# Kernel optimization log

Hardware: AMD Instinct MI355X
Metric: run time of the kernel (lower is better)

Reference implementation:

```python
import jax, jax.numpy as jnp
import numpy as np

N = 100000   # nodes
E = 1600000  # edges (avg degree 16)
D = 64       # input_dim
H = 64       # hidden_dim
C = 40       # num_classes
K = 2        # x_steps (KProp)


def setup_inputs() -> dict:
    key = jax.random.key(0)
    ks = jax.random.split(key, 8)
    x = jax.random.normal(ks[0], (N, D), dtype=jnp.float32)
    edge_src = jax.random.randint(ks[1], (E,), 0, N, dtype=jnp.int32)
    edge_dst = jax.random.randint(ks[2], (E,), 0, N, dtype=jnp.int32)
    def lin(k, fi, fo):
        b = 1.0 / np.sqrt(fi)
        return jax.random.uniform(k, (fi, fo), jnp.float32, -b, b)
    Wl1 = lin(ks[3], D, H)  # SAGEConv1 neighbor weight
    Wr1 = lin(ks[4], D, H)  # SAGEConv1 root weight
    b1 = jnp.zeros((H,), jnp.float32)
    Wl2 = lin(ks[5], H, C)
    Wr2 = lin(ks[6], H, C)
    b2 = jnp.zeros((C,), jnp.float32)
    return {"x": x, "Wl1": Wl1, "Wr1": Wr1, "b1": b1,
            "Wl2": Wl2, "Wr2": Wr2, "b2": b2,
            "edge_src": edge_src, "edge_dst": edge_dst}


def reference(x, Wl1, Wr1, b1, Wl2, Wr2, b2, edge_src, edge_dst):
    ones = jnp.ones((edge_src.shape[0],), x.dtype)
    deg = jax.ops.segment_sum(ones, edge_dst, num_segments=N)  # in-degree (adj_t row sums)
    # gcn_norm without self loops: w_e = deg[dst]^-1/2 * deg[src]^-1/2 (inf -> 0)
    dis = jnp.where(deg > 0, jax.lax.rsqrt(jnp.maximum(deg, 1.0)), 0.0)
    w = dis[edge_dst] * dis[edge_src]
    # KProp: K steps of normalized sparse matmul, 'add' aggregation
    h = x
    for _ in range(K):
        h = jax.ops.segment_sum(h[edge_src] * w[:, None], edge_dst, num_segments=N)
    cnt = jnp.maximum(deg, 1.0)[:, None]  # mean-aggr denominator (0-row safe)
    # SAGEConv1: lin_l(mean_neighbors) + lin_r(root), then selu (dropout p=0)
    agg1 = jax.ops.segment_sum(h[edge_src], edge_dst, num_segments=N) / cnt
    h1 = jax.nn.selu(agg1 @ Wl1 + h @ Wr1 + b1)
    # SAGEConv2
    agg2 = jax.ops.segment_sum(h1[edge_src], edge_dst, num_segments=N) / cnt
    out = agg2 @ Wl2 + h1 @ Wr2 + b2
    return jax.nn.softmax(out, axis=1)
```

## Files before the change

kernel.cpp:

```cpp
#include <hip/hip_runtime.h>
#include <hip/hip_bf16.h>
#include <math.h>


#define RFL(x) __builtin_amdgcn_readfirstlane(x)
#define BK_SHIFT 10
#define MAXBUCK 256

typedef short bf16x8 __attribute__((ext_vector_type(8)));
typedef _Float16 f16x8 __attribute__((ext_vector_type(8)));
typedef float f32x4 __attribute__((ext_vector_type(4)));
typedef unsigned short ushort8v __attribute__((ext_vector_type(8)));

__device__ __forceinline__ float bf2f(unsigned short u) {
    return __uint_as_float((unsigned)u << 16);
}
__device__ __forceinline__ unsigned short f2bf(float f) {
    __hip_bfloat16 b = __float2bfloat16(f);
    return *reinterpret_cast<unsigned short*>(&b);
}
__device__ __forceinline__ unsigned short f2h(float f) {
    _Float16 h = (_Float16)f;
    return *reinterpret_cast<unsigned short*>(&h);
}


__global__ __launch_bounds__(256) void partition_kernel(const int* __restrict__ src,
                                                        const int* __restrict__ dst,
                                                        int* __restrict__ bcursor,
                                                        unsigned int* __restrict__ temp,
                                                        int e, int nbuck, int cap) {
    __shared__ int bc[MAXBUCK];
    int t = threadIdx.x;
    int chunk = (e + gridDim.x - 1) / gridDim.x;
    int base = blockIdx.x * chunk;
    int cnt = e - base;
    if (cnt > chunk) cnt = chunk;
    if (cnt < 0) cnt = 0;
    for (int j = t; j < nbuck; j += 256) bc[j] = 0;
    __syncthreads();
    for (int i = t; i < cnt; i += 256) {
        int d = dst[base + i];
        atomicAdd(&bc[d >> BK_SHIFT], 1);
    }
    __syncthreads();
    for (int j = t; j < nbuck; j += 256) {
        int c = bc[j];
        bc[j] = (c > 0) ? (atomicAdd(&bcursor[j], c) + j * cap) : 0;
    }
    __syncthreads();
    for (int i = t; i < cnt; i += 256) {
        int s = src[base + i];
        int d = dst[base + i];
        int bk = d >> BK_SHIFT;
        int p = atomicAdd(&bc[bk], 1);
        if (p < (bk + 1) * cap) temp[p] = ((unsigned int)s << BK_SHIFT) | (unsigned int)(d & 1023);
    }
}

__global__ __launch_bounds__(256) void bucket_csr_kernel(const unsigned int* __restrict__ temp,
                                                         const int* __restrict__ bcursor,
                                                         int* __restrict__ row_ptr,
                                                         float* __restrict__ dis,
                                                         float* __restrict__ cnt_inv,
                                                         int* __restrict__ csr_src,
                                                         int n, int cap, int nbuck, int e) {
    __shared__ int cnt3[1024];
    __shared__ int part[256];
    int b = blockIdx.x;
    int t = threadIdx.x;
    int nbeg = b << BK_SHIFT;
    int cj = 0;
    if (t < nbuck) {
        cj = bcursor[t];
        if (cj > cap) cj = cap;
    }
    part[t] = cj;
    __syncthreads();
    for (int off = 1; off < 256; off <<= 1) {
        int u = (t >= off) ? part[t - off] : 0;
        __syncthreads();
        part[t] += u;
        __syncthreads();
    }
    int cntb = bcursor[b];
    if (cntb > cap) cntb = cap;
    int bbase = part[b] - cntb;
    __syncthreads();
    for (int i = t; i < 1024; i += 256) cnt3[i] = 0;
    __syncthreads();
    const unsigned int* tb = temp + (size_t)b * cap;
    for (int i = t; i < cntb; i += 256) {
        atomicAdd(&cnt3[tb[i] & 1023u], 1);
    }
    __syncthreads();
    int d0 = cnt3[t * 4 + 0], d1 = cnt3[t * 4 + 1], d2 = cnt3[t * 4 + 2], d3 = cnt3[t * 4 + 3];
    int run = d0 + d1 + d2 + d3;
    int dd[4] = {d0, d1, d2, d3};
#pragma unroll
    for (int k = 0; k < 4; ++k) {
        int node = nbeg + t * 4 + k;
        if (node < n) {
            float fd = (float)dd[k];
            dis[node] = (dd[k] > 0) ? rsqrtf(fd) : 0.0f;
            cnt_inv[node] = 1.0f / fmaxf(fd, 1.0f);
        }
    }
    __syncthreads();
    part[t] = run;
    __syncthreads();
    for (int off = 1; off < 256; off <<= 1) {
        int u = (t >= off) ? part[t - off] : 0;
        __syncthreads();
        part[t] += u;
        __syncthreads();
    }
    int ex = part[t] - run;
    int oo[4];
    oo[0] = ex; oo[1] = ex + d0; oo[2] = ex + d0 + d1; oo[3] = ex + d0 + d1 + d2;
#pragma unroll
    for (int k = 0; k < 4; ++k) {
        cnt3[t * 4 + k] = oo[k];
        int node = nbeg + t * 4 + k;
        if (node < n) row_ptr[node] = bbase + oo[k];
    }
    if (b == nbuck - 1 && t == 0) row_ptr[n] = e;
    __syncthreads();
    for (int i = t; i < cntb; i += 256) {
        unsigned int ed = tb[i];
        int pos = atomicAdd(&cnt3[ed & 1023u], 1);
        csr_src[bbase + pos] = (int)(ed >> BK_SHIFT);
    }
}

__global__ void f2bf_scale_kernel(const float4* __restrict__ in, ushort4* __restrict__ out,
                                  const float* __restrict__ dis, int n4) {
    int i = blockIdx.x * blockDim.x + threadIdx.x;
    if (i < n4) {
        float d = dis[i >> 4];
        float4 v = in[i];
        ushort4 u;
        u.x = f2bf(v.x * d); u.y = f2bf(v.y * d); u.z = f2bf(v.z * d); u.w = f2bf(v.w * d);
        out[i] = u;
    }
}

template <int POW>
__global__ __launch_bounds__(256) void prop4bf_kernel(const ushort4* __restrict__ in4u,
                                                      ushort4* __restrict__ out4u,
                                                      const int* __restrict__ row_ptr,
                                                      const int* __restrict__ csr_src,
                                                      const float* __restrict__ dis,
                                                      int n) {
    int lane = threadIdx.x & 63;
    int g = lane >> 4;
    int l = lane & 15;
    int node = RFL(blockIdx.x * 4 + (threadIdx.x >> 6));
    if (node >= n) return;
    int beg = row_ptr[node];
    int end = row_ptr[node + 1];
    float4 acc = make_float4(0.f, 0.f, 0.f, 0.f);
    int j = beg;
    for (; j + 16 <= end; j += 16) {
        int s[4];
        ushort4 u[4];
#pragma unroll
        for (int q = 0; q < 4; ++q) s[q] = csr_src[j + q * 4 + g];
#pragma unroll
        for (int q = 0; q < 4; ++q) u[q] = in4u[(size_t)s[q] * 16 + l];
#pragma unroll
        for (int q = 0; q < 4; ++q) {
            acc.x += bf2f(u[q].x);
            acc.y += bf2f(u[q].y);
            acc.z += bf2f(u[q].z);
            acc.w += bf2f(u[q].w);
        }
    }
    for (; j + 8 <= end; j += 8) {
        int s[2];
        ushort4 u[2];
#pragma unroll
        for (int q = 0; q < 2; ++q) s[q] = csr_src[j + q * 4 + g];
#pragma unroll
        for (int q = 0; q < 2; ++q) u[q] = in4u[(size_t)s[q] * 16 + l];
#pragma unroll
        for (int q = 0; q < 2; ++q) {
            acc.x += bf2f(u[q].x);
            acc.y += bf2f(u[q].y);
            acc.z += bf2f(u[q].z);
            acc.w += bf2f(u[q].w);
        }
    }
    for (; j < end; j += 4) {
        int idx = j + g;
        bool valid = idx < end;
        int s = csr_src[valid ? idx : (end - 1)];
        float w = valid ? 1.0f : 0.0f;
        ushort4 u = in4u[(size_t)s * 16 + l];
        acc.x += w * bf2f(u.x);
        acc.y += w * bf2f(u.y);
        acc.z += w * bf2f(u.z);
        acc.w += w * bf2f(u.w);
    }
    acc.x += __shfl_xor(acc.x, 16); acc.x += __shfl_xor(acc.x, 32);
    acc.y += __shfl_xor(acc.y, 16); acc.y += __shfl_xor(acc.y, 32);
    acc.z += __shfl_xor(acc.z, 16); acc.z += __shfl_xor(acc.z, 32);
    acc.w += __shfl_xor(acc.w, 16); acc.w += __shfl_xor(acc.w, 32);
    if (g == 0) {
        float d = dis[node];
        float sc = (POW == 2) ? d * d : d;
        ushort4 o;
        o.x = f2bf(acc.x * sc);
        o.y = f2bf(acc.y * sc);
        o.z = f2bf(acc.z * sc);
        o.w = f2bf(acc.w * sc);
        out4u[(size_t)node * 16 + l] = o;
    }
}

__global__ __launch_bounds__(256) void prop_mean_bf_kernel(const ushort4* __restrict__ in4u,
                                                           ushort4* __restrict__ out4u,
                                                           const int* __restrict__ row_ptr,
                                                           const int* __restrict__ csr_src,
                                                           const float* __restrict__ cnt_inv,
                                                           const float4* __restrict__ r4,
                                                           const float4* __restrict__ b4,
                                                           int n) {
    int lane = threadIdx.x & 63;
    int g = lane >> 4;
    int l = lane & 15;
    int node = RFL(blockIdx.x * 4 + (threadIdx.x >> 6));
    if (node >= n) return;
    int beg = row_ptr[node];
    int end = row_ptr[node + 1];
    float4 acc = make_float4(0.f, 0.f, 0.f, 0.f);
    int j = beg;
    for (; j + 16 <= end; j += 16) {
        int s[4];
        ushort4 u[4];
#pragma unroll
        for (int q = 0; q < 4; ++q) s[q] = csr_src[j + q * 4 + g];
#pragma unroll
        for (int q = 0; q < 4; ++q) u[q] = in4u[(size_t)s[q] * 16 + l];
#pragma unroll
        for (int q = 0; q < 4; ++q) {
            acc.x += bf2f(u[q].x);
            acc.y += bf2f(u[q].y);
            acc.z += bf2f(u[q].z);
            acc.w += bf2f(u[q].w);
        }
    }
    for (; j + 8 <= end; j += 8) {
        int s[2];
        ushort4 u[2];
#pragma unroll
        for (int q = 0; q < 2; ++q) s[q] = csr_src[j + q * 4 + g];
#pragma unroll
        for (int q = 0; q < 2; ++q) u[q] = in4u[(size_t)s[q] * 16 + l];
#pragma unroll
        for (int q = 0; q < 2; ++q) {
            acc.x += bf2f(u[q].x);
            acc.y += bf2f(u[q].y);
            acc.z += bf2f(u[q].z);
            acc.w += bf2f(u[q].w);
        }
    }
    for (; j < end; j += 4) {
        int idx = j + g;
        bool valid = idx < end;
        int s = csr_src[valid ? idx : (end - 1)];
        float w = valid ? 1.0f : 0.0f;
        ushort4 u = in4u[(size_t)s * 16 + l];
        acc.x += w * bf2f(u.x);
        acc.y += w * bf2f(u.y);
        acc.z += w * bf2f(u.z);
        acc.w += w * bf2f(u.w);
    }
    acc.x += __shfl_xor(acc.x, 16); acc.x += __shfl_xor(acc.x, 32);
    acc.y += __shfl_xor(acc.y, 16); acc.y += __shfl_xor(acc.y, 32);
    acc.z += __shfl_xor(acc.z, 16); acc.z += __shfl_xor(acc.z, 32);
    acc.w += __shfl_xor(acc.w, 16); acc.w += __shfl_xor(acc.w, 32);
    if (g == 0) {
        float sc = cnt_inv[node];
        float4 ra = r4[(size_t)node * 16 + l];
        float4 bb = b4[l];
        const float scale = 1.0507009873554805f;
        const float alpha = 1.6732632423543772f;
        float t0 = acc.x * sc + ra.x + bb.x;
        float t1 = acc.y * sc + ra.y + bb.y;
        float t2 = acc.z * sc + ra.z + bb.z;
        float t3 = acc.w * sc + ra.w + bb.w;
        t0 = scale * (t0 > 0.0f ? t0 : alpha * expm1f(t0));
        t1 = scale * (t1 > 0.0f ? t1 : alpha * expm1f(t1));
        t2 = scale * (t2 > 0.0f ? t2 : alpha * expm1f(t2));
        t3 = scale * (t3 > 0.0f ? t3 : alpha * expm1f(t3));
        ushort4 o;
        o.x = f2bf(t0); o.y = f2bf(t1); o.z = f2bf(t2); o.w = f2bf(t3);
        out4u[(size_t)node * 16 + l] = o;
    }
}

__global__ __launch_bounds__(256) void prop_mean_plain_kernel(const ushort4* __restrict__ in4u,
                                                              ushort4* __restrict__ out4u,
                                                              const int* __restrict__ row_ptr,
                                                              const int* __restrict__ csr_src,
                                                              const float* __restrict__ cnt_inv,
                                                              int n) {
    int lane = threadIdx.x & 63;
    int g = lane >> 4;
    int l = lane & 15;
    int node = RFL(blockIdx.x * 4 + (threadIdx.x >> 6));
    if (node >= n) return;
    int beg = row_ptr[node];
    int end = row_ptr[node + 1];
    float4 acc = make_float4(0.f, 0.f, 0.f, 0.f);
    int j = beg;
    for (; j + 16 <= end; j += 16) {
        int s[4];
        ushort4 u[4];
#pragma unroll
        for (int q = 0; q < 4; ++q) s[q] = csr_src[j + q * 4 + g];
#pragma unroll
        for (int q = 0; q < 4; ++q) u[q] = in4u[(size_t)s[q] * 16 + l];
#pragma unroll
        for (int q = 0; q < 4; ++q) {
            acc.x += bf2f(u[q].x);
            acc.y += bf2f(u[q].y);
            acc.z += bf2f(u[q].z);
            acc.w += bf2f(u[q].w);
        }
    }
    for (; j + 8 <= end; j += 8) {
        int s[2];
        ushort4 u[2];
#pragma unroll
        for (int q = 0; q < 2; ++q) s[q] = csr_src[j + q * 4 + g];
#pragma unroll
        for (int q = 0; q < 2; ++q) u[q] = in4u[(size_t)s[q] * 16 + l];
#pragma unroll
        for (int q = 0; q < 2; ++q) {
            acc.x += bf2f(u[q].x);
            acc.y += bf2f(u[q].y);
            acc.z += bf2f(u[q].z);
            acc.w += bf2f(u[q].w);
        }
    }
    for (; j < end; j += 4) {
        int idx = j + g;
        bool valid = idx < end;
        int s = csr_src[valid ? idx : (end - 1)];
        float w = valid ? 1.0f : 0.0f;
        ushort4 u = in4u[(size_t)s * 16 + l];
        acc.x += w * bf2f(u.x);
        acc.y += w * bf2f(u.y);
        acc.z += w * bf2f(u.z);
        acc.w += w * bf2f(u.w);
    }
    acc.x += __shfl_xor(acc.x, 16); acc.x += __shfl_xor(acc.x, 32);
    acc.y += __shfl_xor(acc.y, 16); acc.y += __shfl_xor(acc.y, 32);
    acc.z += __shfl_xor(acc.z, 16); acc.z += __shfl_xor(acc.z, 32);
    acc.w += __shfl_xor(acc.w, 16); acc.w += __shfl_xor(acc.w, 32);
    if (g == 0) {
        float sc = cnt_inv[node];
        ushort4 o;
        o.x = f2h(acc.x * sc);
        o.y = f2h(acc.y * sc);
        o.z = f2h(acc.z * sc);
        o.w = f2h(acc.w * sc);
        out4u[(size_t)node * 16 + l] = o;
    }
}

template <int OC>
__global__ __launch_bounds__(256) void gemm_mfma_kernel(const unsigned short* __restrict__ in,
                                                        const float* __restrict__ Wl,
                                                        const float* __restrict__ Wr,
                                                        const float* __restrict__ bias,
                                                        __hip_bfloat16* __restrict__ outL,
                                                        float* __restrict__ outR,
                                                        int n, int add_bias) {
    constexpr int HC = OC / 2;
    constexpr int NF = OC / 16;
    __shared__ unsigned short sA[64 * 64];
    __shared__ unsigned short sBh[OC * 64];
    __shared__ unsigned short sBr[OC * 64];
    int t = threadIdx.x;
    int blk = blockIdx.x;

#pragma unroll
    for (int i = 0; i < 2; ++i) {
        int idx = i * 256 + t;
        int m = idx >> 3;
        int kb = idx & 7;
        int node = blk * 64 + m;
        if (node >= n) node = n - 1;
        ushort8v v = *reinterpret_cast<const ushort8v*>(in + (size_t)node * 64 + kb * 8);
        *reinterpret_cast<ushort8v*>(&sA[m * 64 + ((kb ^ (m & 7)) << 3)]) = v;
    }
    for (int idx = t; idx < 64 * OC; idx += 256) {
        int k = idx / OC;
        int c = idx - k * OC;
        float v = (c < HC) ? Wl[k * HC + c] : Wr[k * HC + (c - HC)];
        unsigned short hi = f2bf(v);
        unsigned short re = f2bf(v - bf2f(hi));
        int pos = c * 64 + (((k >> 3) ^ (c & 7)) << 3) + (k & 7);
        sBh[pos] = hi;
        sBr[pos] = re;
    }
    __syncthreads();

    int w = t >> 6;
    int lane = t & 63;
    int r = lane & 15;
    int q = lane >> 4;
    int m = w * 16 + r;
    bf16x8 A0 = *reinterpret_cast<const bf16x8*>(&sA[m * 64 + (((0 + q) ^ (r & 7)) << 3)]);
    bf16x8 A1 = *reinterpret_cast<const bf16x8*>(&sA[m * 64 + (((4 + q) ^ (r & 7)) << 3)]);

    f32x4 acc[NF];
#pragma unroll
    for (int c = 0; c < NF; ++c) acc[c] = (f32x4)(0.0f);

#pragma unroll
    for (int c = 0; c < NF; ++c) {
        int cb = c * 16 + r;
        bf16x8 B0 = *reinterpret_cast<const bf16x8*>(&sBh[cb * 64 + (((0 + q) ^ (r & 7)) << 3)]);
        bf16x8 B1 = *reinterpret_cast<const bf16x8*>(&sBh[cb * 64 + (((4 + q) ^ (r & 7)) << 3)]);
        bf16x8 R0 = *reinterpret_cast<const bf16x8*>(&sBr[cb * 64 + (((0 + q) ^ (r & 7)) << 3)]);
        bf16x8 R1 = *reinterpret_cast<const bf16x8*>(&sBr[cb * 64 + (((4 + q) ^ (r & 7)) << 3)]);
        acc[c] = __builtin_amdgcn_mfma_f32_16x16x32_bf16(A0, B0, acc[c], 0, 0, 0);
        acc[c] = __builtin_amdgcn_mfma_f32_16x16x32_bf16(A1, B1, acc[c], 0, 0, 0);
        acc[c] = __builtin_amdgcn_mfma_f32_16x16x32_bf16(A0, R0, acc[c], 0, 0, 0);
        acc[c] = __builtin_amdgcn_mfma_f32_16x16x32_bf16(A1, R1, acc[c], 0, 0, 0);
    }

#pragma unroll
    for (int c = 0; c < NF; ++c) {
        int col = c * 16 + r;
#pragma unroll
        for (int j = 0; j < 4; ++j) {
            int node = blk * 64 + w * 16 + q * 4 + j;
            if (node < n) {
                float v = acc[c][j];
                if (col < HC) {
                    outL[(size_t)node * HC + col] = __float2bfloat16(v);
                } else {
                    outR[(size_t)node * HC + (col - HC)] = v + (add_bias ? bias[col - HC] : 0.0f);
                }
            }
        }
    }
}

__global__ __launch_bounds__(256) void gemm2_softmax_kernel(const unsigned short* __restrict__ aggf,
                                                            const unsigned short* __restrict__ h1,
                                                            const float* __restrict__ Wl2,
                                                            const float* __restrict__ Wr2,
                                                            const float* __restrict__ b2,
                                                            float* __restrict__ out,
                                                            int n) {
    __shared__ unsigned short sA[64 * 128];
    __shared__ unsigned short sBh[48 * 128];
    __shared__ unsigned short sBr[48 * 128];
    int t = threadIdx.x;
    int blk = blockIdx.x;

#pragma unroll
    for (int i = 0; i < 4; ++i) {
        int idx = i * 256 + t;
        int m = idx >> 4;
        int kb = idx & 15;
        int node = blk * 64 + m;
        if (node >= n) node = n - 1;
        const unsigned short* srcp = (kb < 8) ? aggf : h1;
        ushort8v v = *reinterpret_cast<const ushort8v*>(srcp + (size_t)node * 64 + (kb & 7) * 8);
        *reinterpret_cast<ushort8v*>(&sA[m * 128 + ((kb ^ (m & 7)) << 3)]) = v;
    }
    for (int idx = t; idx < 48 * 128; idx += 256) {
        int k = idx / 48;
        int c = idx - k * 48;
        float v = 0.0f;
        if (c < 40) v = (k < 64) ? Wl2[k * 40 + c] : Wr2[(k - 64) * 40 + c];
        unsigned short hi, re;
        if (k < 64) {
            _Float16 h = (_Float16)v;
            float res = v - (float)h;
            _Float16 h2 = (_Float16)res;
            hi = *reinterpret_cast<unsigned short*>(&h);
            re = *reinterpret_cast<unsigned short*>(&h2);
        } else {
            hi = f2bf(v);
            re = f2bf(v - bf2f(hi));
        }
        int pos = c * 128 + (((k >> 3) ^ (c & 7)) << 3) + (k & 7);
        sBh[pos] = hi;
        sBr[pos] = re;
    }
    __syncthreads();

    int w = t >> 6;
    int lane = t & 63;
    int r = lane & 15;
    int q = lane >> 4;
    int m = w * 16 + r;
    f16x8  Af0 = *reinterpret_cast<const f16x8*>(&sA[m * 128 + (((0 + q) ^ (r & 7)) << 3)]);
    f16x8  Af1 = *reinterpret_cast<const f16x8*>(&sA[m * 128 + (((4 + q) ^ (r & 7)) << 3)]);
    bf16x8 Ab0 = *reinterpret_cast<const bf16x8*>(&sA[m * 128 + (((8 + q) ^ (r & 7)) << 3)]);
    bf16x8 Ab1 = *reinterpret_cast<const bf16x8*>(&sA[m * 128 + (((12 + q) ^ (r & 7)) << 3)]);

    f32x4 acc[3];
#pragma unroll
    for (int c = 0; c < 3; ++c) acc[c] = (f32x4)(0.0f);

#pragma unroll
    for (int c = 0; c < 3; ++c) {
        int cb = c * 16 + r;
        const unsigned short* bh = &sBh[cb * 128];
        const unsigned short* br = &sBr[cb * 128];
        f16x8  Bf0 = *reinterpret_cast<const f16x8*>(&bh[(((0 + q) ^ (r & 7)) << 3)]);
        f16x8  Bf1 = *reinterpret_cast<const f16x8*>(&bh[(((4 + q) ^ (r & 7)) << 3)]);
        bf16x8 Bb0 = *reinterpret_cast<const bf16x8*>(&bh[(((8 + q) ^ (r & 7)) << 3)]);
        bf16x8 Bb1 = *reinterpret_cast<const bf16x8*>(&bh[(((12 + q) ^ (r & 7)) << 3)]);
        f16x8  Rf0 = *reinterpret_cast<const f16x8*>(&br[(((0 + q) ^ (r & 7)) << 3)]);
        f16x8  Rf1 = *reinterpret_cast<const f16x8*>(&br[(((4 + q) ^ (r & 7)) << 3)]);
        bf16x8 Rb0 = *reinterpret_cast<const bf16x8*>(&br[(((8 + q) ^ (r & 7)) << 3)]);
        bf16x8 Rb1 = *reinterpret_cast<const bf16x8*>(&br[(((12 + q) ^ (r & 7)) << 3)]);
        acc[c] = __builtin_amdgcn_mfma_f32_16x16x32_f16(Af0, Bf0, acc[c], 0, 0, 0);
        acc[c] = __builtin_amdgcn_mfma_f32_16x16x32_f16(Af1, Bf1, acc[c], 0, 0, 0);
        acc[c] = __builtin_amdgcn_mfma_f32_16x16x32_f16(Af0, Rf0, acc[c], 0, 0, 0);
        acc[c] = __builtin_amdgcn_mfma_f32_16x16x32_f16(Af1, Rf1, acc[c], 0, 0, 0);
        acc[c] = __builtin_amdgcn_mfma_f32_16x16x32_bf16(Ab0, Bb0, acc[c], 0, 0, 0);
        acc[c] = __builtin_amdgcn_mfma_f32_16x16x32_bf16(Ab1, Bb1, acc[c], 0, 0, 0);
        acc[c] = __builtin_amdgcn_mfma_f32_16x16x32_bf16(Ab0, Rb0, acc[c], 0, 0, 0);
        acc[c] = __builtin_amdgcn_mfma_f32_16x16x32_bf16(Ab1, Rb1, acc[c], 0, 0, 0);
    }

    float bv0 = b2[r];
    float bv1 = b2[16 + r];
    float bv2 = (r < 8) ? b2[32 + r] : 0.0f;
#pragma unroll
    for (int j = 0; j < 4; ++j) {
        int node = blk * 64 + w * 16 + q * 4 + j;
        float v0 = acc[0][j] + bv0;
        float v1 = acc[1][j] + bv1;
        float v2 = (r < 8) ? (acc[2][j] + bv2) : -INFINITY;
        float mx = fmaxf(fmaxf(v0, v1), v2);
        mx = fmaxf(mx, __shfl_xor(mx, 1));
        mx = fmaxf(mx, __shfl_xor(mx, 2));
        mx = fmaxf(mx, __shfl_xor(mx, 4));
        mx = fmaxf(mx, __shfl_xor(mx, 8));
        float e0 = __expf(v0 - mx);
        float e1 = __expf(v1 - mx);
        float e2 = (r < 8) ? __expf(v2 - mx) : 0.0f;
        float s = e0 + e1 + e2;
        s += __shfl_xor(s, 1);
        s += __shfl_xor(s, 2);
        s += __shfl_xor(s, 4);
        s += __shfl_xor(s, 8);
        if (node < n) {
            float inv = 1.0f / s;
            out[(size_t)node * 40 + r] = e0 * inv;
            out[(size_t)node * 40 + 16 + r] = e1 * inv;
            if (r < 8) out[(size_t)node * 40 + 32 + r] = e2 * inv;
        }
    }
}


extern "C" void kernel_launch(void* const* d_in, const int* in_sizes, int n_in,
                              void* d_out, int out_size, void* d_ws, size_t ws_size,
                              hipStream_t stream) {
    const float* x   = (const float*)d_in[0];
    const float* Wl1 = (const float*)d_in[1];
    const float* Wr1 = (const float*)d_in[2];
    const float* b1  = (const float*)d_in[3];
    const float* Wl2 = (const float*)d_in[4];
    const float* Wr2 = (const float*)d_in[5];
    const float* b2  = (const float*)d_in[6];
    const int* edge_src = (const int*)d_in[7];
    const int* edge_dst = (const int*)d_in[8];
    float* out = (float*)d_out;

    const int N = in_sizes[0] / 64;
    const int E = in_sizes[7];
    const int NBUCK = (N + (1 << BK_SHIFT) - 1) >> BK_SHIFT;
    size_t buf_bytes = (size_t)N * 64 * 4;
    int cap = E / NBUCK + E / (2 * NBUCK) + 1024;
    int cap_max = (int)(buf_bytes / ((size_t)NBUCK * 4));
    if (cap > cap_max) cap = cap_max;

    size_t off = 0;
    auto carve = [&](size_t bytes) -> void* {
        void* p = (char*)d_ws + off;
        off = (off + bytes + 255) & ~(size_t)255;
        return p;
    };
    int*          row_ptr = (int*)carve((size_t)(N + 1) * 4);
    int*          bcursor = (int*)carve((size_t)NBUCK * 4);
    float*        dis     = (float*)carve((size_t)N * 4);
    float*        cnt_inv = (float*)carve((size_t)N * 4);
    int*          csr_src = (int*)carve((size_t)E * 4);
    char*         bufA    = (char*)carve(buf_bytes);
    char*         bufB    = (char*)carve(buf_bytes);
    float*        bufC    = (float*)carve(buf_bytes);
    unsigned int* temp    = (unsigned int*)bufC;
    (void)ws_size;

    unsigned short* xb    = (unsigned short*)bufA;
    unsigned short* p0b   = (unsigned short*)(bufA + buf_bytes / 2);
    unsigned short* hb    = (unsigned short*)bufB;
    unsigned short* t1b   = (unsigned short*)bufA;
    unsigned short* h1b   = (unsigned short*)bufB;
    unsigned short* agg2b = (unsigned short*)(bufA + buf_bytes / 2);

    const int nb_node = (N + 3) / 4;
    const int nb_gemm = (N + 63) / 64;
    const int n4 = N * 64 / 4;

    hipMemsetAsync(bcursor, 0, (size_t)NBUCK * 4, stream);
    partition_kernel<<<256, 256, 0, stream>>>(edge_src, edge_dst, bcursor, temp, E, NBUCK, cap);
    bucket_csr_kernel<<<NBUCK, 256, 0, stream>>>(temp, bcursor, row_ptr, dis, cnt_inv,
                                                 csr_src, N, cap, NBUCK, E);

    f2bf_scale_kernel<<<(n4 + 255) / 256, 256, 0, stream>>>((const float4*)x, (ushort4*)xb,
                                                            dis, n4);
    prop4bf_kernel<2><<<nb_node, 256, 0, stream>>>((const ushort4*)xb, (ushort4*)p0b,
                                                   row_ptr, csr_src, dis, N);
    prop4bf_kernel<1><<<nb_node, 256, 0, stream>>>((const ushort4*)p0b, (ushort4*)hb,
                                                   row_ptr, csr_src, dis, N);
    gemm_mfma_kernel<128><<<nb_gemm, 256, 0, stream>>>(hb, Wl1, Wr1, nullptr,
                                                       (__hip_bfloat16*)t1b, bufC, N, 0);
    prop_mean_bf_kernel<<<nb_node, 256, 0, stream>>>((const ushort4*)t1b, (ushort4*)h1b,
                                                     row_ptr, csr_src, cnt_inv,
                                                     (const float4*)bufC, (const float4*)b1, N);
    prop_mean_plain_kernel<<<nb_node, 256, 0, stream>>>((const ushort4*)h1b, (ushort4*)agg2b,
                                                        row_ptr, csr_src, cnt_inv, N);
    gemm2_softmax_kernel<<<nb_gemm, 256, 0, stream>>>(agg2b, h1b, Wl2, Wr2, b2, out, N);
}
```

Before: 370.2 us.

## Aggregate before first SAGE linear layer and fuse selu into GEMM

Reorders layer 1 so the mean aggregation runs on the propagated features first (stored as fp16), followed by a single fused GEMM over the concatenated [agg, h] inputs with bias and selu applied in its epilogue. This removes the fp32 root-projection buffer round-trip and the separate selu-fused propagation kernel. Gather width stays 64 features either way, so the saving comes mainly from less intermediate traffic. The cost is a larger shared-memory GEMM with K=128 and mixed f16/bf16 MFMA, which may lower occupancy.

Measured after the change: 366.8 us. Within noise of the previous version (-0.9%).

```diff
diff --git a/kernel.cpp b/kernel.cpp
--- a/kernel.cpp
+++ b/kernel.cpp
@@ -218,88 +218,6 @@
     }
 }
 
-__global__ __launch_bounds__(256) void prop_mean_bf_kernel(const ushort4* __restrict__ in4u,
-                                                           ushort4* __restrict__ out4u,
-                                                           const int* __restrict__ row_ptr,
-                                                           const int* __restrict__ csr_src,
-                                                           const float* __restrict__ cnt_inv,
-                                                           const float4* __restrict__ r4,
-                                                           const float4* __restrict__ b4,
-                                                           int n) {
-    int lane = threadIdx.x & 63;
-    int g = lane >> 4;
-    int l = lane & 15;
-    int node = RFL(blockIdx.x * 4 + (threadIdx.x >> 6));
-    if (node >= n) return;
-    int beg = row_ptr[node];
-    int end = row_ptr[node + 1];
-    float4 acc = make_float4(0.f, 0.f, 0.f, 0.f);
-    int j = beg;
-    for (; j + 16 <= end; j += 16) {
-        int s[4];
-        ushort4 u[4];
-#pragma unroll
-        for (int q = 0; q < 4; ++q) s[q] = csr_src[j + q * 4 + g];
-#pragma unroll
-        for (int q = 0; q < 4; ++q) u[q] = in4u[(size_t)s[q] * 16 + l];
-#pragma unroll
-        for (int q = 0; q < 4; ++q) {
-            acc.x += bf2f(u[q].x);
-            acc.y += bf2f(u[q].y);
-            acc.z += bf2f(u[q].z);
-            acc.w += bf2f(u[q].w);
-        }
-    }
-    for (; j + 8 <= end; j += 8) {
-        int s[2];
-        ushort4 u[2];
-#pragma unroll
-        for (int q = 0; q < 2; ++q) s[q] = csr_src[j + q * 4 + g];
-#pragma unroll
-        for (int q = 0; q < 2; ++q) u[q] = in4u[(size_t)s[q] * 16 + l];
-#pragma unroll
-        for (int q = 0; q < 2; ++q) {
-            acc.x += bf2f(u[q].x);
-            acc.y += bf2f(u[q].y);
-            acc.z += bf2f(u[q].z);
-            acc.w += bf2f(u[q].w);
-        }
-    }
-    for (; j < end; j += 4) {
-        int idx = j + g;
-        bool valid = idx < end;
-        int s = csr_src[valid ? idx : (end - 1)];
-        float w = valid ? 1.0f : 0.0f;
-        ushort4 u = in4u[(size_t)s * 16 + l];
-        acc.x += w * bf2f(u.x);
-        acc.y += w * bf2f(u.y);
-        acc.z += w * bf2f(u.z);
-        acc.w += w * bf2f(u.w);
-    }
-    acc.x += __shfl_xor(acc.x, 16); acc.x += __shfl_xor(acc.x, 32);
-    acc.y += __shfl_xor(acc.y, 16); acc.y += __shfl_xor(acc.y, 32);
-    acc.z += __shfl_xor(acc.z, 16); acc.z += __shfl_xor(acc.z, 32);
-    acc.w += __shfl_xor(acc.w, 16); acc.w += __shfl_xor(acc.w, 32);
-    if (g == 0) {
-        float sc = cnt_inv[node];
-        float4 ra = r4[(size_t)node * 16 + l];
-        float4 bb = b4[l];
-        const float scale = 1.0507009873554805f;
-        const float alpha = 1.6732632423543772f;
-        float t0 = acc.x * sc + ra.x + bb.x;
-        float t1 = acc.y * sc + ra.y + bb.y;
-        float t2 = acc.z * sc + ra.z + bb.z;
-        float t3 = acc.w * sc + ra.w + bb.w;
-        t0 = scale * (t0 > 0.0f ? t0 : alpha * expm1f(t0));
-        t1 = scale * (t1 > 0.0f ? t1 : alpha * expm1f(t1));
-        t2 = scale * (t2 > 0.0f ? t2 : alpha * expm1f(t2));
-        t3 = scale * (t3 > 0.0f ? t3 : alpha * expm1f(t3));
-        ushort4 o;
-        o.x = f2bf(t0); o.y = f2bf(t1); o.z = f2bf(t2); o.w = f2bf(t3);
-        out4u[(size_t)node * 16 + l] = o;
-    }
-}
-
 __global__ __launch_bounds__(256) void prop_mean_plain_kernel(const ushort4* __restrict__ in4u,
                                                               ushort4* __restrict__ out4u,
                                                               const int* __restrict__ row_ptr,
@@ -371,39 +289,46 @@
     }
 }
 
-template <int OC>
-__global__ __launch_bounds__(256) void gemm_mfma_kernel(const unsigned short* __restrict__ in,
-                                                        const float* __restrict__ Wl,
-                                                        const float* __restrict__ Wr,
-                                                        const float* __restrict__ bias,
-                                                        __hip_bfloat16* __restrict__ outL,
-                                                        float* __restrict__ outR,
-                                                        int n, int add_bias) {
-    constexpr int HC = OC / 2;
-    constexpr int NF = OC / 16;
-    __shared__ unsigned short sA[64 * 64];
-    __shared__ unsigned short sBh[OC * 64];
-    __shared__ unsigned short sBr[OC * 64];
+__global__ __launch_bounds__(256) void gemm1_selu_kernel(const unsigned short* __restrict__ aggf,
+                                                         const unsigned short* __restrict__ h,
+                                                         const float* __restrict__ Wl1,
+                                                         const float* __restrict__ Wr1,
+                                                         const float* __restrict__ b1,
+                                                         unsigned short* __restrict__ h1,
+                                                         int n) {
+    __shared__ unsigned short sA[64 * 128];
+    __shared__ unsigned short sBh[64 * 128];
+    __shared__ unsigned short sBr[64 * 128];
     int t = threadIdx.x;
     int blk = blockIdx.x;
 
 #pragma unroll
-    for (int i = 0; i < 2; ++i) {
+    for (int i = 0; i < 4; ++i) {
         int idx = i * 256 + t;
-        int m = idx >> 3;
-        int kb = idx & 7;
+        int m = idx >> 4;
+        int kb = idx & 15;
         int node = blk * 64 + m;
         if (node >= n) node = n - 1;
-        ushort8v v = *reinterpret_cast<const ushort8v*>(in + (size_t)node * 64 + kb * 8);
-        *reinterpret_cast<ushort8v*>(&sA[m * 64 + ((kb ^ (m & 7)) << 3)]) = v;
-    }
-    for (int idx = t; idx < 64 * OC; idx += 256) {
-        int k = idx / OC;
-        int c = idx - k * OC;
-        float v = (c < HC) ? Wl[k * HC + c] : Wr[k * HC + (c - HC)];
-        unsigned short hi = f2bf(v);
-        unsigned short re = f2bf(v - bf2f(hi));
-        int pos = c * 64 + (((k >> 3) ^ (c & 7)) << 3) + (k & 7);
+        const unsigned short* srcp = (kb < 8) ? aggf : h;
+        ushort8v v = *reinterpret_cast<const ushort8v*>(srcp + (size_t)node * 64 + (kb & 7) * 8);
+        *reinterpret_cast<ushort8v*>(&sA[m * 128 + ((kb ^ (m & 7)) << 3)]) = v;
+    }
+    for (int idx = t; idx < 64 * 128; idx += 256) {
+        int k = idx >> 6;
+        int c = idx & 63;
+        float v = (k < 64) ? Wl1[k * 64 + c] : Wr1[(k - 64) * 64 + c];
+        unsigned short hi, re;
+        if (k < 64) {
+            _Float16 hh = (_Float16)v;
+            float res = v - (float)hh;
+            _Float16 h2 = (_Float16)res;
+            hi = *reinterpret_cast<unsigned short*>(&hh);
+            re = *reinterpret_cast<unsigned short*>(&h2);
+        } else {
+            hi = f2bf(v);
+            re = f2bf(v - bf2f(hi));
+        }
+        int pos = c * 128 + (((k >> 3) ^ (c & 7)) << 3) + (k & 7);
         sBh[pos] = hi;
         sBr[pos] = re;
     }
@@ -414,39 +339,51 @@
     int r = lane & 15;
     int q = lane >> 4;
     int m = w * 16 + r;
-    bf16x8 A0 = *reinterpret_cast<const bf16x8*>(&sA[m * 64 + (((0 + q) ^ (r & 7)) << 3)]);
-    bf16x8 A1 = *reinterpret_cast<const bf16x8*>(&sA[m * 64 + (((4 + q) ^ (r & 7)) << 3)]);
-
-    f32x4 acc[NF];
-#pragma unroll
-    for (int c = 0; c < NF; ++c) acc[c] = (f32x4)(0.0f);
-
-#pragma unroll
-    for (int c = 0; c < NF; ++c) {
+    f16x8  Af0 = *reinterpret_cast<const f16x8*>(&sA[m * 128 + (((0 + q) ^ (r & 7)) << 3)]);
+    f16x8  Af1 = *reinterpret_cast<const f16x8*>(&sA[m * 128 + (((4 + q) ^ (r & 7)) << 3)]);
+    bf16x8 Ab0 = *reinterpret_cast<const bf16x8*>(&sA[m * 128 + (((8 + q) ^ (r & 7)) << 3)]);
+    bf16x8 Ab1 = *reinterpret_cast<const bf16x8*>(&sA[m * 128 + (((12 + q) ^ (r & 7)) << 3)]);
+
+    f32x4 acc[4];
+#pragma unroll
+    for (int c = 0; c < 4; ++c) acc[c] = (f32x4)(0.0f);
+
+#pragma unroll
+    for (int c = 0; c < 4; ++c) {
         int cb = c * 16 + r;
-        bf16x8 B0 = *reinterpret_cast<const bf16x8*>(&sBh[cb * 64 + (((0 + q) ^ (r & 7)) << 3)]);
-        bf16x8 B1 = *reinterpret_cast<const bf16x8*>(&sBh[cb * 64 + (((4 + q) ^ (r & 7)) << 3)]);
-        bf16x8 R0 = *reinterpret_cast<const bf16x8*>(&sBr[cb * 64 + (((0 + q) ^ (r & 7)) << 3)]);
-        bf16x8 R1 = *reinterpret_cast<const bf16x8*>(&sBr[cb * 64 + (((4 + q) ^ (r & 7)) << 3)]);
-        acc[c] = __builtin_amdgcn_mfma_f32_16x16x32_bf16(A0, B0, acc[c], 0, 0, 0);
-        acc[c] = __builtin_amdgcn_mfma_f32_16x16x32_bf16(A1, B1, acc[c], 0, 0, 0);
-        acc[c] = __builtin_amdgcn_mfma_f32_16x16x32_bf16(A0, R0, acc[c], 0, 0, 0);
-        acc[c] = __builtin_amdgcn_mfma_f32_16x16x32_bf16(A1, R1, acc[c], 0, 0, 0);
-    }
-
-#pragma unroll
-    for (int c = 0; c < NF; ++c) {
+        const unsigned short* bh = &sBh[cb * 128];
+        const unsigned short* br = &sBr[cb * 128];
+        f16x8  Bf0 = *reinterpret_cast<const f16x8*>(&bh[(((0 + q) ^ (r & 7)) << 3)]);
+        f16x8  Bf1 = *reinterpret_cast<const f16x8*>(&bh[(((4 + q) ^ (r & 7)) << 3)]);
+        bf16x8 Bb0 = *reinterpret_cast<const bf16x8*>(&bh[(((8 + q) ^ (r & 7)) << 3)]);
+        bf16x8 Bb1 = *reinterpret_cast<const bf16x8*>(&bh[(((12 + q) ^ (r & 7)) << 3)]);
+        f16x8  Rf0 = *reinterpret_cast<const f16x8*>(&br[(((0 + q) ^ (r & 7)) << 3)]);
+        f16x8  Rf1 = *reinterpret_cast<const f16x8*>(&br[(((4 + q) ^ (r & 7)) << 3)]);
+        bf16x8 Rb0 = *reinterpret_cast<const bf16x8*>(&br[(((8 + q) ^ (r & 7)) << 3)]);
+        bf16x8 Rb1 = *reinterpret_cast<const bf16x8*>(&br[(((12 + q) ^ (r & 7)) << 3)]);
+        acc[c] = __builtin_amdgcn_mfma_f32_16x16x32_f16(Af0, Bf0, acc[c], 0, 0, 0);
+        acc[c] = __builtin_amdgcn_mfma_f32_16x16x32_f16(Af1, Bf1, acc[c], 0, 0, 0);
+        acc[c] = __builtin_amdgcn_mfma_f32_16x16x32_f16(Af0, Rf0, acc[c], 0, 0, 0);
+        acc[c] = __builtin_amdgcn_mfma_f32_16x16x32_f16(Af1, Rf1, acc[c], 0, 0, 0);
+        acc[c] = __builtin_amdgcn_mfma_f32_16x16x32_bf16(Ab0, Bb0, acc[c], 0, 0, 0);
+        acc[c] = __builtin_amdgcn_mfma_f32_16x16x32_bf16(Ab1, Bb1, acc[c], 0, 0, 0);
+        acc[c] = __builtin_amdgcn_mfma_f32_16x16x32_bf16(Ab0, Rb0, acc[c], 0, 0, 0);
+        acc[c] = __builtin_amdgcn_mfma_f32_16x16x32_bf16(Ab1, Rb1, acc[c], 0, 0, 0);
+    }
+
+    const float scale = 1.0507009873554805f;
+    const float alpha = 1.6732632423543772f;
+#pragma unroll
+    for (int c = 0; c < 4; ++c) {
         int col = c * 16 + r;
+        float bv = b1[col];
 #pragma unroll
         for (int j = 0; j < 4; ++j) {
             int node = blk * 64 + w * 16 + q * 4 + j;
             if (node < n) {
-                float v = acc[c][j];
-                if (col < HC) {
-                    outL[(size_t)node * HC + col] = __float2bfloat16(v);
-                } else {
-                    outR[(size_t)node * HC + (col - HC)] = v + (add_bias ? bias[col - HC] : 0.0f);
-                }
+                float v = acc[c][j] + bv;
+                v = scale * (v > 0.0f ? v : alpha * expm1f(v));
+                h1[(size_t)node * 64 + col] = f2bf(v);
             }
         }
     }
@@ -606,12 +543,12 @@
     unsigned int* temp    = (unsigned int*)bufC;
     (void)ws_size;
 
-    unsigned short* xb    = (unsigned short*)bufA;
-    unsigned short* p0b   = (unsigned short*)(bufA + buf_bytes / 2);
-    unsigned short* hb    = (unsigned short*)bufB;
-    unsigned short* t1b   = (unsigned short*)bufA;
-    unsigned short* h1b   = (unsigned short*)bufB;
-    unsigned short* agg2b = (unsigned short*)(bufA + buf_bytes / 2);
+    unsigned short* xb  = (unsigned short*)bufA;
+    unsigned short* p0b = (unsigned short*)(bufA + buf_bytes / 2);
+    unsigned short* hb  = (unsigned short*)bufB;
+    unsigned short* hm  = (unsigned short*)bufA;
+    unsigned short* h1b = (unsigned short*)(bufA + buf_bytes / 2);
+    unsigned short* hm2 = (unsigned short*)(bufB + buf_bytes / 2);
 
     const int nb_node = (N + 3) / 4;
     const int nb_gemm = (N + 63) / 64;
@@ -628,12 +565,10 @@
                                                    row_ptr, csr_src, dis, N);
     prop4bf_kernel<1><<<nb_node, 256, 0, stream>>>((const ushort4*)p0b, (ushort4*)hb,
                                                    row_ptr, csr_src, dis, N);
-    gemm_mfma_kernel<128><<<nb_gemm, 256, 0, stream>>>(hb, Wl1, Wr1, nullptr,
-                                                       (__hip_bfloat16*)t1b, bufC, N, 0);
-    prop_mean_bf_kernel<<<nb_node, 256, 0, stream>>>((const ushort4*)t1b, (ushort4*)h1b,
-                                                     row_ptr, csr_src, cnt_inv,
-                                                     (const float4*)bufC, (const float4*)b1, N);
-    prop_mean_plain_kernel<<<nb_node, 256, 0, stream>>>((const ushort4*)h1b, (ushort4*)agg2b,
+    prop_mean_plain_kernel<<<nb_node, 256, 0, stream>>>((const ushort4*)hb, (ushort4*)hm,
                                                         row_ptr, csr_src, cnt_inv, N);
-    gemm2_softmax_kernel<<<nb_gemm, 256, 0, stream>>>(agg2b, h1b, Wl2, Wr2, b2, out, N);
-}
+    gemm1_selu_kernel<<<nb_gemm, 256, 0, stream>>>(hm, hb, Wl1, Wr1, b1, h1b, N);
+    prop_mean_plain_kernel<<<nb_node, 256, 0, stream>>>((const ushort4*)h1b, (ushort4*)hm2,
+                                                        row_ptr, csr_src, cnt_inv, N);
+    gemm2_softmax_kernel<<<nb_gemm, 256, 0, stream>>>(hm2, h1b, Wl2, Wr2, b2, out, N);
+}
```
